# Performance work log

Hardware: AMD Instinct MI355X
Metric: run time of the kernel (lower is better)

## Reference

```python
import jax, jax.numpy as jnp
import numpy as np
from jax import lax

B, T, E, H, L = 32, 512, 1024, 1024, 128


def setup_inputs() -> dict:
    key = jax.random.key(0)
    ks = jax.random.split(key, 25)
    s = 0.02  # small init scale for stable tanh/sigmoid

    def p(k, shape):
        return jax.random.normal(k, shape, jnp.float32) * s

    return {
        "x": jax.random.normal(ks[0], (B, T, E), jnp.float32),
        "eps": jax.random.normal(ks[1], (B, L), jnp.float32),
        # linear1 / linear2 (torch convention: W is [out, in])
        "W1": p(ks[2], (H, E)), "b1": jnp.zeros((H,), jnp.float32),
        "W2": p(ks[3], (H, H)), "b2": jnp.zeros((H,), jnp.float32),
        # encoder GRU (gates ordered r,z,n as in torch)
        "Wih_e": p(ks[4], (3 * H, H)), "Whh_e": p(ks[5], (3 * H, H)),
        "bih_e": jnp.zeros((3 * H,), jnp.float32), "bhh_e": jnp.zeros((3 * H,), jnp.float32),
        # decoder GRU
        "Wih_d": p(ks[6], (3 * H, H)), "Whh_d": p(ks[7], (3 * H, H)),
        "bih_d": jnp.zeros((3 * H,), jnp.float32), "bhh_d": jnp.zeros((3 * H,), jnp.float32),
        # VAE heads
        "Wm": p(ks[8], (L, H)), "bm": jnp.zeros((L,), jnp.float32),
        "Wv": p(ks[9], (L, H)), "bv": jnp.zeros((L,), jnp.float32),
        "Wl": p(ks[10], (H, L)), "bl": jnp.zeros((H,), jnp.float32),
        # output layer (H -> E)
        "Wo": p(ks[11], (E, H)), "bo": jnp.zeros((E,), jnp.float32),
        "lengths": jax.random.randint(ks[12], (B,), 1, T + 1, jnp.int32),
    }


def _gru(xs, h0, Wih, Whh, bih, bhh, lengths):
    """torch-style GRU over padded batch xs:[B,T,H].
    Emulates pack_padded_sequence: h frozen and outputs zeroed for t >= length.
    Returns (outputs [B,T,H], final hidden [B,H])."""
    Tn = xs.shape[1]

    def step(h, inp):
        xt, t = inp  # xt:[B,H]
        gi = xt @ Wih.T + bih          # [B,3H]
        gh = h @ Whh.T + bhh           # [B,3H]
        ir, iz, inn = jnp.split(gi, 3, axis=-1)
        hr, hz, hn = jnp.split(gh, 3, axis=-1)
        r = jax.nn.sigmoid(ir + hr)
        zg = jax.nn.sigmoid(iz + hz)
        n = jnp.tanh(inn + r * hn)
        hnew = (1.0 - zg) * n + zg * h
        valid = (t < lengths)[:, None]
        hout = jnp.where(valid, hnew, h)
        yout = jnp.where(valid, hnew, 0.0)  # pad_packed padding_value=0.0
        return hout, yout

    hT, ys = lax.scan(step, h0, (xs.transpose(1, 0, 2), jnp.arange(Tn)))
    return ys.transpose(1, 0, 2), hT


def reference(x, eps, W1, b1, W2, b2, Wih_e, Whh_e, bih_e, bhh_e,
              Wih_d, Whh_d, bih_d, bhh_d, Wm, bm, Wv, bv, Wl, bl, Wo, bo,
              lengths):
    # pad() sorts the batch by descending length (stable) for packing
    sorted_idx = jnp.argsort(-lengths)
    rev_idx = jnp.argsort(sorted_idx)
    xs = x[sorted_idx]            # sorted padded input
    ls = lengths[sorted_idx]

    # shared input projection linear2(relu(linear1(.)))  (decoder dropout is eval-mode identity)
    proj = jnp.maximum(xs @ W1.T + b1, 0.0) @ W2.T + b2   # [B,T,H]

    h0 = jnp.zeros((xs.shape[0], H), proj.dtype)
    _, h_enc = _gru(proj, h0, Wih_e, Whh_e, bih_e, bhh_e, ls)  # [B,H]

    mean = h_enc @ Wm.T + bm
    logv = h_enc @ Wv.T + bv
    z = eps * jnp.exp(0.5 * logv) + mean                   # [B,L], sorted order
    dec_h0 = z @ Wl.T + bl                                 # [B,H]

    ys, _ = _gru(proj, dec_h0, Wih_d, Whh_d, bih_d, bhh_d, ls)  # [B,T,H]
    outputs_layer = ys[rev_idx] @ Wo.T + bo                # unsorted, [B,T,E]

    return (x, outputs_layer, mean, logv, z)
```

## Files before the change

### kernel.cpp

```cpp
#include <hip/hip_runtime.h>
#include <stdint.h>

#define B_  32
#define T_  512
#define E_  1024
#define H_  1024
#define L_  128
#define BT  (B_*T_)
#define G3  (3*H_)

typedef float f32x4 __attribute__((ext_vector_type(4)));
typedef short bf16x8 __attribute__((ext_vector_type(8)));

__device__ __forceinline__ unsigned short f2bf(float f) {
  unsigned u = __float_as_uint(f);
  u = (u + 0x7fffu + ((u >> 16) & 1u)) >> 16;
  return (unsigned short)u;
}
__device__ __forceinline__ float bf2f(unsigned short s) {
  return __uint_as_float(((unsigned)s) << 16);
}

__global__ void k_f2bf(const float* __restrict__ in, unsigned short* __restrict__ out, int n) {
  int i = (blockIdx.x * blockDim.x + threadIdx.x) * 4;
  if (i >= n) return;
  float4 v = *(const float4*)(in + i);
  unsigned lo = (unsigned)f2bf(v.x) | ((unsigned)f2bf(v.y) << 16);
  unsigned hi = (unsigned)f2bf(v.z) | ((unsigned)f2bf(v.w) << 16);
  *(uint2*)(out + i) = make_uint2(lo, hi);
}

template<int OUT_F32, int RELU>
__global__ __launch_bounds__(256)
void k_gemm(const unsigned short* __restrict__ A, const unsigned short* __restrict__ W,
            const float* __restrict__ bias, void* __restrict__ Cc,
            int M, int N, int K)
{
  __shared__ __align__(16) unsigned short As[128 * 64];
  __shared__ __align__(16) unsigned short Bs[128 * 64];
  const int m0 = blockIdx.x * 128, n0 = blockIdx.y * 128;
  const int tid = threadIdx.x;
  const int lane = tid & 63, wv = tid >> 6;
  const int wr = wv >> 1, wc = wv & 1;
  f32x4 acc[4][4] = {};

  for (int k0 = 0; k0 < K; k0 += 64) {
#pragma unroll
    for (int i = 0; i < 4; ++i) {
      int o = tid * 16 + i * 4096;
      int r = o >> 7;
      int cb = o & 127;
      const unsigned short* ga = A + (size_t)(m0 + r) * K + k0 + (cb >> 1);
      const unsigned short* gb = W + (size_t)(n0 + r) * K + k0 + (cb >> 1);
      __builtin_amdgcn_global_load_lds((const __attribute__((address_space(1))) void*)ga,
          (__attribute__((address_space(3))) void*)((char*)As + o), 16, 0, 0);
      __builtin_amdgcn_global_load_lds((const __attribute__((address_space(1))) void*)gb,
          (__attribute__((address_space(3))) void*)((char*)Bs + o), 16, 0, 0);
    }
    __syncthreads();
#pragma unroll
    for (int kk = 0; kk < 2; ++kk) {
      bf16x8 af[4], bfr[4];
#pragma unroll
      for (int m = 0; m < 4; ++m)
        af[m] = *(const bf16x8*)(As + (wr * 64 + m * 16 + (lane & 15)) * 64 + kk * 32 + (lane >> 4) * 8);
#pragma unroll
      for (int n = 0; n < 4; ++n)
        bfr[n] = *(const bf16x8*)(Bs + (wc * 64 + n * 16 + (lane & 15)) * 64 + kk * 32 + (lane >> 4) * 8);
#pragma unroll
      for (int m = 0; m < 4; ++m)
#pragma unroll
        for (int n = 0; n < 4; ++n)
          acc[m][n] = __builtin_amdgcn_mfma_f32_16x16x32_bf16(af[m], bfr[n], acc[m][n], 0, 0, 0);
    }
    __syncthreads();
  }
#pragma unroll
  for (int m = 0; m < 4; ++m) {
    int row0 = m0 + wr * 64 + m * 16 + (lane >> 4) * 4;
#pragma unroll
    for (int n = 0; n < 4; ++n) {
      int col = n0 + wc * 64 + n * 16 + (lane & 15);
      float bvv = bias[col];
#pragma unroll
      for (int q = 0; q < 4; ++q) {
        float v = acc[m][n][q] + bvv;
        if (RELU) v = fmaxf(v, 0.f);
        size_t idx = (size_t)(row0 + q) * N + col;
        if (OUT_F32) ((float*)Cc)[idx] = v;
        else ((unsigned short*)Cc)[idx] = f2bf(v);
      }
    }
  }
}

template<int IS_DEC>
__global__ __launch_bounds__(384, 2)
void k_gru(const unsigned short* __restrict__ gi,
           const unsigned short* __restrict__ Whhb,
           const float* __restrict__ bhh,
           const int* __restrict__ lengths,
           const float* __restrict__ h0,
           float* __restrict__ hT,
           unsigned short* __restrict__ ys,
           unsigned short* __restrict__ hbuf,
           unsigned* __restrict__ flags)
{
  const int wg = blockIdx.x;
  const int U0 = wg * 16;
  const int tid = threadIdx.x;
  const int lane = tid & 63, wv = tid >> 6;
  const int mt = wv & 1, g = wv >> 1;

  __shared__ float gh_lds[32][49];
  __shared__ float h_master[32][16];
  __shared__ float bhh_s[48];
  __shared__ int len_s[32];

  if (tid < 32) len_s[tid] = lengths[tid];
  if (tid < 48) bhh_s[tid] = bhh[(tid >> 4) * 1024 + U0 + (tid & 15)];

  bf16x8 bfrag[32];
  {
    const unsigned short* wrow = Whhb + (size_t)(g * 1024 + U0 + (lane & 15)) * 1024 + ((lane >> 4) * 8);
#pragma unroll
    for (int kc = 0; kc < 32; ++kc)
      bfrag[kc] = *(const bf16x8*)(wrow + kc * 32);
  }

  const int gb = tid >> 3, gu2 = tid & 7;
  const unsigned short* gibase = gi + (size_t)gb * T_ * G3 + U0 + gu2 * 2;
  unsigned vr_c = 0, vz_c = 0, vn_c = 0, vr_n = 0, vz_n = 0, vn_n = 0;
  if (tid < 256) {
    vr_c = *(const unsigned*)(gibase);
    vz_c = *(const unsigned*)(gibase + 1024);
    vn_c = *(const unsigned*)(gibase + 2048);
  }

  for (int p = tid; p < 512; p += 384) {
    int b = p >> 4, u = p & 15;
    float h = IS_DEC ? h0[b * 1024 + U0 + u] : 0.f;
    h_master[b][u] = h;
    hbuf[b * 1024 + U0 + u] = f2bf(h);
  }
  __syncthreads();
  if (tid == 0)
    __hip_atomic_store(flags + wg * 16, 1u, __ATOMIC_RELEASE, __HIP_MEMORY_SCOPE_AGENT);

  for (int t = 0; t < T_; ++t) {
    if (tid < 256 && t + 1 < T_) {
      const unsigned short* p = gibase + (size_t)(t + 1) * G3;
      vr_n = *(const unsigned*)(p);
      vz_n = *(const unsigned*)(p + 1024);
      vn_n = *(const unsigned*)(p + 2048);
    }
    if (wv == 0) {
      unsigned* fp = flags + lane * 16;
      while (__hip_atomic_load(fp, __ATOMIC_RELAXED, __HIP_MEMORY_SCOPE_AGENT) < (unsigned)(t + 1)) {}
      __builtin_amdgcn_fence(__ATOMIC_ACQUIRE, "agent");
    }
    __syncthreads();

    const unsigned short* hb = hbuf + (t & 1) * (32 * 1024);
    f32x4 a0 = {0.f, 0.f, 0.f, 0.f}, a1 = {0.f, 0.f, 0.f, 0.f};
    const unsigned short* arow = hb + (size_t)(mt * 16 + (lane & 15)) * 1024 + ((lane >> 4) * 8);
#pragma unroll
    for (int kc = 0; kc < 32; kc += 2) {
      bf16x8 f0 = *(const bf16x8*)(arow + kc * 32);
      bf16x8 f1 = *(const bf16x8*)(arow + kc * 32 + 32);
      a0 = __builtin_amdgcn_mfma_f32_16x16x32_bf16(f0, bfrag[kc], a0, 0, 0, 0);
      a1 = __builtin_amdgcn_mfma_f32_16x16x32_bf16(f1, bfrag[kc + 1], a1, 0, 0, 0);
    }
#pragma unroll
    for (int q = 0; q < 4; ++q)
      gh_lds[mt * 16 + (lane >> 4) * 4 + q][g * 16 + (lane & 15)] = a0[q] + a1[q];
    __syncthreads();

    if (tid < 256) {
      int b = gb, u2 = gu2;
      int valid = t < len_s[b];
      unsigned hw = 0, yw = 0;
#pragma unroll
      for (int j = 0; j < 2; ++j) {
        int u = u2 * 2 + j;
        float ir  = bf2f((unsigned short)(j ? (vr_c >> 16) : (vr_c & 0xffff)));
        float iz  = bf2f((unsigned short)(j ? (vz_c >> 16) : (vz_c & 0xffff)));
        float in_ = bf2f((unsigned short)(j ? (vn_c >> 16) : (vn_c & 0xffff)));
        float gr = gh_lds[b][u]      + bhh_s[u];
        float gz = gh_lds[b][16 + u] + bhh_s[16 + u];
        float gn = gh_lds[b][32 + u] + bhh_s[32 + u];
        float rr = 1.f / (1.f + expf(-(ir + gr)));
        float zz = 1.f / (1.f + expf(-(iz + gz)));
        float nn = tanhf(in_ + rr * gn);
        float hp = h_master[b][u];
        float hn = valid ? ((1.f - zz) * nn + zz * hp) : hp;
        h_master[b][u] = hn;
        unsigned short hb16 = f2bf(hn);
        hw |= ((unsigned)hb16) << (16 * j);
        if (IS_DEC) { unsigned short yb = valid ? hb16 : (unsigned short)0; yw |= ((unsigned)yb) << (16 * j); }
      }
      unsigned* hnext = (unsigned*)(hbuf + ((t + 1) & 1) * (32 * 1024));
      hnext[(b * 1024 + U0 + u2 * 2) >> 1] = hw;
      if (IS_DEC) ((unsigned*)ys)[((size_t)(b * T_ + t) * 1024 + U0 + u2 * 2) >> 1] = yw;
    }
    __syncthreads();
    if (tid == 0)
      __hip_atomic_store(flags + wg * 16, (unsigned)(t + 2), __ATOMIC_RELEASE, __HIP_MEMORY_SCOPE_AGENT);
    vr_c = vr_n; vz_c = vz_n; vn_c = vn_n;
  }

  if (!IS_DEC && tid < 256) {
    int b = tid >> 3, u2 = tid & 7;
    hT[b * 1024 + U0 + u2 * 2]     = h_master[b][u2 * 2];
    hT[b * 1024 + U0 + u2 * 2 + 1] = h_master[b][u2 * 2 + 1];
  }
}

__global__ __launch_bounds__(256)
void k_mid(const float* __restrict__ h_enc,
           const float* __restrict__ Wm, const float* __restrict__ bm,
           const float* __restrict__ Wv, const float* __restrict__ bv,
           const float* __restrict__ Wl, const float* __restrict__ bl,
           const float* __restrict__ eps, const int* __restrict__ lengths,
           float* __restrict__ out_mean, float* __restrict__ out_logv,
           float* __restrict__ out_z, float* __restrict__ dec_h0)
{
  const int b = blockIdx.x;
  const int tid = threadIdx.x;
  __shared__ float h_s[1024];
  __shared__ float mean_s[128], logv_s[128], z_s[128];
  __shared__ int pos_s;
  for (int i = tid; i < 1024; i += 256) h_s[i] = h_enc[b * 1024 + i];
  if (tid == 0) {
    int lb = lengths[b], r = 0;
    for (int j = 0; j < 32; ++j) {
      int lj = lengths[j];
      r += (lj > lb) || (lj == lb && j < b);
    }
    pos_s = r;
  }
  __syncthreads();
  {
    const float* wrow = (tid < 128) ? (Wm + tid * 1024) : (Wv + (tid - 128) * 1024);
    float s = 0.f;
    for (int k = 0; k < 1024; ++k) s += h_s[k] * wrow[k];
    s += (tid < 128) ? bm[tid] : bv[tid - 128];
    if (tid < 128) mean_s[tid] = s; else logv_s[tid - 128] = s;
  }
  __syncthreads();
  int pos = pos_s;
  if (tid < 128) {
    float zv = eps[pos * 128 + tid] * expf(0.5f * logv_s[tid]) + mean_s[tid];
    z_s[tid] = zv;
    out_mean[pos * 128 + tid] = mean_s[tid];
    out_logv[pos * 128 + tid] = logv_s[tid];
    out_z[pos * 128 + tid]    = zv;
  }
  __syncthreads();
  for (int h = tid; h < 1024; h += 256) {
    float s = bl[h];
    const float* w = Wl + h * 128;
    for (int k = 0; k < 128; ++k) s += z_s[k] * w[k];
    dec_h0[b * 1024 + h] = s;
  }
}

extern "C" void kernel_launch(void* const* d_in, const int* in_sizes, int n_in,
                              void* d_out, int out_size, void* d_ws, size_t ws_size,
                              hipStream_t stream)
{
  const float* x     = (const float*)d_in[0];
  const float* eps   = (const float*)d_in[1];
  const float* W1    = (const float*)d_in[2];
  const float* b1    = (const float*)d_in[3];
  const float* W2    = (const float*)d_in[4];
  const float* b2    = (const float*)d_in[5];
  const float* Wih_e = (const float*)d_in[6];
  const float* Whh_e = (const float*)d_in[7];
  const float* bih_e = (const float*)d_in[8];
  const float* bhh_e = (const float*)d_in[9];
  const float* Wih_d = (const float*)d_in[10];
  const float* Whh_d = (const float*)d_in[11];
  const float* bih_d = (const float*)d_in[12];
  const float* bhh_d = (const float*)d_in[13];
  const float* Wm    = (const float*)d_in[14];
  const float* bm    = (const float*)d_in[15];
  const float* Wv    = (const float*)d_in[16];
  const float* bv    = (const float*)d_in[17];
  const float* Wl    = (const float*)d_in[18];
  const float* bl    = (const float*)d_in[19];
  const float* Wo    = (const float*)d_in[20];
  const float* bo    = (const float*)d_in[21];
  const int* lengths = (const int*)d_in[22];

  char* ws = (char*)d_ws;
  unsigned short* xb    = (unsigned short*)(ws + 0);
  unsigned short* proj  = (unsigned short*)(ws + 33554432);
  unsigned short* gi    = (unsigned short*)(ws + 67108864);
  unsigned short* W1b   = (unsigned short*)(ws + 167772160);
  unsigned short* W2b   = (unsigned short*)(ws + 169869312);
  unsigned short* Wiheb = (unsigned short*)(ws + 171966464);
  unsigned short* Wihdb = (unsigned short*)(ws + 178257920);
  unsigned short* Whheb = (unsigned short*)(ws + 184549376);
  unsigned short* Whhdb = (unsigned short*)(ws + 190840832);
  unsigned short* Wob   = (unsigned short*)(ws + 197132288);
  unsigned short* hbuf  = (unsigned short*)(ws + 199229440);
  float* h_enc          = (float*)(ws + 199360512);
  float* dec_h0         = (float*)(ws + 199491584);
  unsigned* bars        = (unsigned*)(ws + 199622656);

  float* out_x    = (float*)d_out;
  float* out_ol   = (float*)d_out + 16777216;
  float* out_mean = (float*)d_out + 2 * 16777216;
  float* out_logv = out_mean + 4096;
  float* out_z    = out_logv + 4096;

  hipMemcpyAsync(out_x, x, (size_t)16777216 * 4, hipMemcpyDeviceToDevice, stream);
  hipMemsetAsync(bars, 0, 8192, stream);

  auto cv = [&](const float* s, unsigned short* d, int n) {
    k_f2bf<<<dim3((n / 4 + 255) / 256), dim3(256), 0, stream>>>(s, d, n);
  };
  cv(x, xb, BT * E_);
  cv(W1, W1b, H_ * E_);
  cv(W2, W2b, H_ * H_);
  cv(Wih_e, Wiheb, G3 * H_);
  cv(Wih_d, Wihdb, G3 * H_);
  cv(Whh_e, Whheb, G3 * H_);
  cv(Whh_d, Whhdb, G3 * H_);
  cv(Wo, Wob, E_ * H_);

  unsigned short* P1 = gi;
  k_gemm<0, 1><<<dim3(BT / 128, H_ / 128), 256, 0, stream>>>(xb, W1b, b1, P1, BT, H_, E_);
  k_gemm<0, 0><<<dim3(BT / 128, H_ / 128), 256, 0, stream>>>(P1, W2b, b2, proj, BT, H_, H_);
  k_gemm<0, 0><<<dim3(BT / 128, G3 / 128), 256, 0, stream>>>(proj, Wiheb, bih_e, gi, BT, G3, H_);
  k_gru<0><<<64, 384, 0, stream>>>(gi, Whheb, bhh_e, lengths, nullptr, h_enc, nullptr, hbuf, bars);
  k_mid<<<32, 256, 0, stream>>>(h_enc, Wm, bm, Wv, bv, Wl, bl, eps, lengths,
                                out_mean, out_logv, out_z, dec_h0);
  k_gemm<0, 0><<<dim3(BT / 128, G3 / 128), 256, 0, stream>>>(proj, Wihdb, bih_d, gi, BT, G3, H_);
  unsigned short* ys = xb;
  k_gru<1><<<64, 384, 0, stream>>>(gi, Whhdb, bhh_d, lengths, dec_h0, nullptr, ys, hbuf, bars + 1024);
  k_gemm<1, 0><<<dim3(BT / 128, E_ / 128), 256, 0, stream>>>(ys, Wob, bo, out_ol, BT, E_, H_);
}
```

Before: 12.69 ms.

## Replace per-step block barrier and release/acquire with per-wave flags and relaxed atomics

```diff
diff --git a/kernel.cpp b/kernel.cpp
--- a/kernel.cpp
+++ b/kernel.cpp
@@ -11,6 +11,7 @@
 
 typedef float f32x4 __attribute__((ext_vector_type(4)));
 typedef short bf16x8 __attribute__((ext_vector_type(8)));
+typedef unsigned long long u64_t;
 
 __device__ __forceinline__ unsigned short f2bf(float f) {
   unsigned u = __float_as_uint(f);
@@ -137,15 +138,21 @@
     vn_c = *(const unsigned*)(gibase + 2048);
   }
 
-  for (int p = tid; p < 512; p += 384) {
-    int b = p >> 4, u = p & 15;
-    float h = IS_DEC ? h0[b * 1024 + U0 + u] : 0.f;
-    h_master[b][u] = h;
-    hbuf[b * 1024 + U0 + u] = f2bf(h);
-  }
-  __syncthreads();
-  if (tid == 0)
-    __hip_atomic_store(flags + wg * 16, 1u, __ATOMIC_RELEASE, __HIP_MEMORY_SCOPE_AGENT);
+  if (tid < 256) {
+    int b = gb, u2 = gu2;
+    float ha = IS_DEC ? h0[b * 1024 + U0 + u2 * 2]     : 0.f;
+    float hbv = IS_DEC ? h0[b * 1024 + U0 + u2 * 2 + 1] : 0.f;
+    h_master[b][u2 * 2]     = ha;
+    h_master[b][u2 * 2 + 1] = hbv;
+    unsigned hw = (unsigned)f2bf(ha) | ((unsigned)f2bf(hbv) << 16);
+    __hip_atomic_store((unsigned*)hbuf + ((b * 1024 + U0 + u2 * 2) >> 1), hw,
+                       __ATOMIC_RELAXED, __HIP_MEMORY_SCOPE_AGENT);
+  }
+  asm volatile("s_waitcnt vmcnt(0)" ::: "memory");
+  if (wv < 4 && lane == 0)
+    __hip_atomic_store(flags + wg * 16 + wv, 1u, __ATOMIC_RELAXED, __HIP_MEMORY_SCOPE_AGENT);
+
+  union F8 { u64_t q[2]; bf16x8 v; };
 
   for (int t = 0; t < T_; ++t) {
     if (tid < 256 && t + 1 < T_) {
@@ -154,22 +161,24 @@
       vz_n = *(const unsigned*)(p + 1024);
       vn_n = *(const unsigned*)(p + 2048);
     }
-    if (wv == 0) {
-      unsigned* fp = flags + lane * 16;
+    if (wv < 4) {
+      const unsigned* fp = flags + lane * 16 + wv;
       while (__hip_atomic_load(fp, __ATOMIC_RELAXED, __HIP_MEMORY_SCOPE_AGENT) < (unsigned)(t + 1)) {}
-      __builtin_amdgcn_fence(__ATOMIC_ACQUIRE, "agent");
     }
     __syncthreads();
 
     const unsigned short* hb = hbuf + (t & 1) * (32 * 1024);
+    const u64_t* arow64 = (const u64_t*)(hb + (size_t)(mt * 16 + (lane & 15)) * 1024 + ((lane >> 4) * 8));
     f32x4 a0 = {0.f, 0.f, 0.f, 0.f}, a1 = {0.f, 0.f, 0.f, 0.f};
-    const unsigned short* arow = hb + (size_t)(mt * 16 + (lane & 15)) * 1024 + ((lane >> 4) * 8);
 #pragma unroll
     for (int kc = 0; kc < 32; kc += 2) {
-      bf16x8 f0 = *(const bf16x8*)(arow + kc * 32);
-      bf16x8 f1 = *(const bf16x8*)(arow + kc * 32 + 32);
-      a0 = __builtin_amdgcn_mfma_f32_16x16x32_bf16(f0, bfrag[kc], a0, 0, 0, 0);
-      a1 = __builtin_amdgcn_mfma_f32_16x16x32_bf16(f1, bfrag[kc + 1], a1, 0, 0, 0);
+      F8 f0, f1;
+      f0.q[0] = __hip_atomic_load(arow64 + kc * 8 + 0, __ATOMIC_RELAXED, __HIP_MEMORY_SCOPE_AGENT);
+      f0.q[1] = __hip_atomic_load(arow64 + kc * 8 + 1, __ATOMIC_RELAXED, __HIP_MEMORY_SCOPE_AGENT);
+      f1.q[0] = __hip_atomic_load(arow64 + kc * 8 + 8, __ATOMIC_RELAXED, __HIP_MEMORY_SCOPE_AGENT);
+      f1.q[1] = __hip_atomic_load(arow64 + kc * 8 + 9, __ATOMIC_RELAXED, __HIP_MEMORY_SCOPE_AGENT);
+      a0 = __builtin_amdgcn_mfma_f32_16x16x32_bf16(f0.v, bfrag[kc], a0, 0, 0, 0);
+      a1 = __builtin_amdgcn_mfma_f32_16x16x32_bf16(f1.v, bfrag[kc + 1], a1, 0, 0, 0);
     }
 #pragma unroll
     for (int q = 0; q < 4; ++q)
@@ -199,18 +208,19 @@
         hw |= ((unsigned)hb16) << (16 * j);
         if (IS_DEC) { unsigned short yb = valid ? hb16 : (unsigned short)0; yw |= ((unsigned)yb) << (16 * j); }
       }
-      unsigned* hnext = (unsigned*)(hbuf + ((t + 1) & 1) * (32 * 1024));
-      hnext[(b * 1024 + U0 + u2 * 2) >> 1] = hw;
+      unsigned* hnext = (unsigned*)hbuf + (((t + 1) & 1) * (32 * 1024) >> 1);
+      __hip_atomic_store(hnext + ((b * 1024 + U0 + u2 * 2) >> 1), hw,
+                         __ATOMIC_RELAXED, __HIP_MEMORY_SCOPE_AGENT);
       if (IS_DEC) ((unsigned*)ys)[((size_t)(b * T_ + t) * 1024 + U0 + u2 * 2) >> 1] = yw;
     }
-    __syncthreads();
-    if (tid == 0)
-      __hip_atomic_store(flags + wg * 16, (unsigned)(t + 2), __ATOMIC_RELEASE, __HIP_MEMORY_SCOPE_AGENT);
+    asm volatile("s_waitcnt vmcnt(0)" ::: "memory");
+    if (wv < 4 && lane == 0)
+      __hip_atomic_store(flags + wg * 16 + wv, (unsigned)(t + 2), __ATOMIC_RELAXED, __HIP_MEMORY_SCOPE_AGENT);
     vr_c = vr_n; vz_c = vz_n; vn_c = vn_n;
   }
 
   if (!IS_DEC && tid < 256) {
-    int b = tid >> 3, u2 = tid & 7;
+    int b = gb, u2 = gu2;
     hT[b * 1024 + U0 + u2 * 2]     = h_master[b][u2 * 2];
     hT[b * 1024 + U0 + u2 * 2 + 1] = h_master[b][u2 * 2 + 1];
   }
```

After: 14.48 ms. +14.0%, slower.
